# Kernel tuning notes

Measured on AMD Instinct MI355X. Metric: run time of the kernel, lower is better.

The kernel has to match this reference:

```python
import jax, jax.numpy as jnp
import numpy as np

N = 50000       # nodes
E = 800000      # edges (avg degree 16)
D_IN = 96
D_OUT = 96
K = 3           # Chebyshev order
EPS = 1e-5      # BatchNorm eps


def setup_inputs() -> dict:
    key = jax.random.key(0)
    k1, k2, k3 = jax.random.split(key, 3)
    x = jax.random.normal(k1, (N, D_IN), dtype=jnp.float32)
    edge_index = jax.random.randint(k2, (2, E), 0, N)
    # ChebConv weights: one [D_IN, D_OUT] matrix per Chebyshev order + shared bias
    W = jax.random.normal(k3, (K, D_IN, D_OUT), dtype=jnp.float32) * (1.0 / np.sqrt(D_IN))
    bias = jnp.zeros((D_OUT,), dtype=jnp.float32)
    # BatchNorm1d affine params
    gamma = jnp.ones((D_OUT,), dtype=jnp.float32)
    beta = jnp.zeros((D_OUT,), dtype=jnp.float32)
    return {"x": x, "edge_index": edge_index, "W": W, "bias": bias,
            "gamma": gamma, "beta": beta}


def _cheb_edge_norm(edge_index, num_nodes):
    # PyG ChebConv.__norm__ with normalization='sym', lambda_max=2.0:
    # L_hat = 2L/lambda_max - I = -D^{-1/2} A D^{-1/2} (self loops removed, diag 0)
    row, col = edge_index[0], edge_index[1]
    w = jnp.where(row != col, 1.0, 0.0)  # remove self loops (weight 0 == removed)
    deg = jax.ops.segment_sum(w, row, num_segments=num_nodes)
    dis = jnp.where(deg > 0, jax.lax.rsqrt(jnp.maximum(deg, 1e-12)), 0.0)
    return -dis[row] * w * dis[col]  # [E]


def reference(x, edge_index, W, bias, gamma, beta):
    row, col = edge_index[0], edge_index[1]
    norm = _cheb_edge_norm(edge_index, N)

    def prop(h):  # sparse L_hat @ h via gather + scatter-add
        return jax.ops.segment_sum(norm[:, None] * h[row], col, num_segments=N)

    # Chebyshev recursion: T0 = x, T1 = L_hat x, Tk = 2 L_hat T_{k-1} - T_{k-2}
    Tx0 = x
    out = Tx0 @ W[0]
    Tx1 = prop(Tx0)
    out = out + Tx1 @ W[1]
    for k in range(2, K):
        Tx2 = 2.0 * prop(Tx1) - Tx0
        out = out + Tx2 @ W[k]
        Tx0, Tx1 = Tx1, Tx2
    out = out + bias

    # BatchNorm1d (training mode: batch stats over nodes, biased variance)
    mean = out.mean(axis=0)
    var = out.var(axis=0)
    return (out - mean) * jax.lax.rsqrt(var + EPS) * gamma + beta
```

## Files before the change

### kernel.cpp

```cpp
#include <hip/hip_runtime.h>

#define N_NODES 50000
#define N_EDGES 800000
#define D 96
#define DH 48
#define CAP 48
#define HG 64
#define W4 (N_NODES / 4)
#define EPS_BN 1e-5f

typedef short bf16x8 __attribute__((ext_vector_type(8)));
typedef float f32x4  __attribute__((ext_vector_type(4)));
union frag_cvt { uint4 u; bf16x8 f; };

__device__ __forceinline__ unsigned pack_bf16(float a, float b) {
    unsigned ua = __float_as_uint(a), ub = __float_as_uint(b);
    ua = (ua + 0x7fffu + ((ua >> 16) & 1u)) >> 16;
    ub = (ub + 0x7fffu + ((ub >> 16) & 1u)) >> 16;
    return (ua & 0xffffu) | (ub << 16);
}
__device__ __forceinline__ unsigned bf16_hi_bits(float a) {
    unsigned u = __float_as_uint(a);
    return (u + 0x7fffu + ((u >> 16) & 1u)) & 0xffff0000u;
}
__device__ __forceinline__ float bf16_lo(unsigned u) { return __uint_as_float(u << 16); }
__device__ __forceinline__ float bf16_hi(unsigned u) { return __uint_as_float(u & 0xffff0000u); }

#define CB ((N_NODES * DH + 1023) / 1024)
__global__ __launch_bounds__(1024) void prep_hist_kernel(
        const int* __restrict__ ei, unsigned* __restrict__ rowpart,
        unsigned* __restrict__ colpart, const float* __restrict__ x,
        unsigned* __restrict__ xh, const float* __restrict__ W,
        unsigned* __restrict__ wswz) {
    if (blockIdx.x < HG) {
        __shared__ unsigned h[W4];
        const int chunk = N_EDGES / HG;
        const int e0 = blockIdx.x * chunk;
        int rs[13], cs[13];
        int n = 0;
        for (int e = e0 + threadIdx.x; e < e0 + chunk; e += 1024, ++n) {
            rs[n] = ei[e];
            cs[n] = ei[N_EDGES + e];
        }
        for (int w = threadIdx.x; w < W4; w += 1024) h[w] = 0;
        __syncthreads();
        for (int i = 0; i < n; ++i)
            if (rs[i] != cs[i]) atomicAdd(&h[rs[i] >> 2], 1u << ((rs[i] & 3) * 8));
        __syncthreads();
        unsigned* rp = rowpart + (size_t)blockIdx.x * W4;
        for (int w = threadIdx.x; w < W4; w += 1024) rp[w] = h[w];
        __syncthreads();
        for (int w = threadIdx.x; w < W4; w += 1024) h[w] = 0;
        __syncthreads();
        for (int i = 0; i < n; ++i)
            if (rs[i] != cs[i]) atomicAdd(&h[cs[i] >> 2], 1u << ((cs[i] & 3) * 8));
        __syncthreads();
        unsigned* cp = colpart + (size_t)blockIdx.x * W4;
        for (int w = threadIdx.x; w < W4; w += 1024) cp[w] = h[w];
    } else if (blockIdx.x < HG + CB) {
        int t = (blockIdx.x - HG) * 1024 + threadIdx.x;
        if (t >= N_NODES * DH) return;
        float2 v = ((const float2*)x)[t];
        xh[t] = pack_bf16(v.x, v.y);
    } else {
        int t = (blockIdx.x - HG - CB) * 1024 + threadIdx.x;
        if (t >= 3 * 3 * 6 * 64) return;
        int lane = t & 63;
        int rest = t >> 6;
        int tile = rest % 6; rest /= 6;
        int q    = rest % 3;
        int s    = rest / 3;
        int n     = tile * 16 + (lane & 15);
        int kbase = q * 32 + (lane >> 4) * 8;
        uint4 u;
        const float* Wk = W + ((size_t)s * D + kbase) * D + n;
        u.x = pack_bf16(Wk[0 * D], Wk[1 * D]);
        u.y = pack_bf16(Wk[2 * D], Wk[3 * D]);
        u.z = pack_bf16(Wk[4 * D], Wk[5 * D]);
        u.w = pack_bf16(Wk[6 * D], Wk[7 * D]);
        ((uint4*)wswz)[t] = u;
    }
}

__global__ void reduce_kernel(unsigned* __restrict__ colpart,
                              const unsigned* __restrict__ rowpart,
                              int* __restrict__ cnt, float* __restrict__ dis,
                              float* __restrict__ stats) {
    if (blockIdx.x == 0 && threadIdx.x < 2 * D) stats[threadIdx.x] = 0.f;
    int w = blockIdx.x * blockDim.x + threadIdx.x;
    if (w >= W4) return;
    unsigned run = 0;
    for (int b = 0; b < HG; ++b) {
        unsigned v = colpart[(size_t)b * W4 + w];
        colpart[(size_t)b * W4 + w] = run;
        run += v;
    }
    int4 c4;
    c4.x = run & 0xffu; c4.y = (run >> 8) & 0xffu;
    c4.z = (run >> 16) & 0xffu; c4.w = run >> 24;
    ((int4*)cnt)[w] = c4;
    unsigned s0 = 0, s1 = 0, s2 = 0, s3 = 0;
    for (int b = 0; b < HG; ++b) {
        unsigned v = rowpart[(size_t)b * W4 + w];
        s0 += v & 0xffu; s1 += (v >> 8) & 0xffu;
        s2 += (v >> 16) & 0xffu; s3 += v >> 24;
    }
    float4 o;
    o.x = s0 ? rsqrtf((float)s0) : 0.f;
    o.y = s1 ? rsqrtf((float)s1) : 0.f;
    o.z = s2 ? rsqrtf((float)s2) : 0.f;
    o.w = s3 ? rsqrtf((float)s3) : 0.f;
    ((float4*)dis)[w] = o;
}

__global__ __launch_bounds__(1024) void place_kernel(const int* __restrict__ ei,
                                                     const unsigned* __restrict__ colpart,
                                                     const float* __restrict__ dis,
                                                     unsigned* __restrict__ ent) {
    __shared__ unsigned h[W4];
    const unsigned* pref = colpart + (size_t)blockIdx.x * W4;
    for (int w = threadIdx.x; w < W4; w += 1024) h[w] = pref[w];
    __syncthreads();
    const int chunk = N_EDGES / HG;
    const int e0 = blockIdx.x * chunk;
    for (int e = e0 + threadIdx.x; e < e0 + chunk; e += 1024) {
        int r = ei[e];
        int c = ei[N_EDGES + e];
        if (r == c) continue;
        float w = -dis[r] * dis[c];
        int sh = (c & 3) * 8;
        unsigned old = atomicAdd(&h[c >> 2], 1u << sh);
        int pos = (old >> sh) & 0xff;
        if (pos < CAP) ent[c * CAP + pos] = bf16_hi_bits(w) | (unsigned)r;
    }
}

template <int MODE>
__global__ __launch_bounds__(256) void prop_gather_kernel(
        const int* __restrict__ cnt_arr, const unsigned* __restrict__ ent,
        const unsigned* __restrict__ hp, const float* __restrict__ x,
        unsigned* __restrict__ out_h) {
    int node = blockIdx.x * 4 + (threadIdx.x >> 6);
    int lane = threadIdx.x & 63;
    if (node >= N_NODES) return;
    const int cl = (lane < DH) ? lane : (lane - DH);
    int cnt = cnt_arr[node]; if (cnt > CAP) cnt = CAP;
    unsigned el = (lane < cnt) ? ent[node * CAP + lane] : 0u;
    float acc0 = 0.f, acc1 = 0.f;
    for (int j = 0; j < cnt; j += 24) {
        unsigned ee[24];
        #pragma unroll
        for (int i = 0; i < 24; ++i)
            ee[i] = (unsigned)__shfl((int)el, j + i, 64);
        unsigned uu[24];
        #pragma unroll
        for (int i = 0; i < 24; ++i)
            uu[i] = hp[(ee[i] & 0xffffu) * DH + cl];
        #pragma unroll
        for (int i = 0; i < 24; ++i) {
            float w = __uint_as_float(ee[i] & 0xffff0000u);
            acc0 = fmaf(w, bf16_lo(uu[i]), acc0);
            acc1 = fmaf(w, bf16_hi(uu[i]), acc1);
        }
    }
    if (lane < DH) {
        if (MODE == 0) {
            out_h[node * DH + cl] = pack_bf16(acc0, acc1);
        } else {
            float2 xv = ((const float2*)x)[node * DH + cl];
            out_h[node * DH + cl] = pack_bf16(fmaf(2.f, acc0, -xv.x),
                                              fmaf(2.f, acc1, -xv.y));
        }
    }
}

__global__ __launch_bounds__(256) void mfma_gemm_kernel(
        const unsigned* __restrict__ xh, const unsigned* __restrict__ t1h,
        const unsigned* __restrict__ t2h, const unsigned* __restrict__ wswz,
        const float* __restrict__ bias, float* __restrict__ out,
        float* __restrict__ stats) {
    const int wave = threadIdx.x >> 6;
    const int lane = threadIdx.x & 63;
    const int m    = lane & 15;
    const int kg   = lane >> 4;
    const int nb   = blockIdx.x * 128 + wave * 32;
    __shared__ float ssum[4][D], ssq[4][D];

    int arow0 = nb + m;       if (arow0 > N_NODES - 1) arow0 = N_NODES - 1;
    int arow1 = nb + 16 + m;  if (arow1 > N_NODES - 1) arow1 = N_NODES - 1;

    const unsigned* bases[3] = {xh, t1h, t2h};

    f32x4 acc[2][6];
    #pragma unroll
    for (int h = 0; h < 2; ++h)
        #pragma unroll
        for (int t = 0; t < 6; ++t) acc[h][t] = (f32x4){0.f, 0.f, 0.f, 0.f};

    #pragma unroll
    for (int s = 0; s < 3; ++s) {
        const unsigned* A0 = bases[s] + (size_t)arow0 * DH + kg * 4;
        const unsigned* A1 = bases[s] + (size_t)arow1 * DH + kg * 4;
        #pragma unroll
        for (int q = 0; q < 3; ++q) {
            frag_cvt a0, a1;
            a0.u = *(const uint4*)(A0 + q * 16);
            a1.u = *(const uint4*)(A1 + q * 16);
            const uint4* Bp = (const uint4*)wswz + (size_t)((s * 3 + q) * 6) * 64 + lane;
            #pragma unroll
            for (int t = 0; t < 6; ++t) {
                frag_cvt b;
                b.u = Bp[t * 64];
                acc[0][t] = __builtin_amdgcn_mfma_f32_16x16x32_bf16(a0.f, b.f, acc[0][t], 0, 0, 0);
                acc[1][t] = __builtin_amdgcn_mfma_f32_16x16x32_bf16(a1.f, b.f, acc[1][t], 0, 0, 0);
            }
        }
    }

    #pragma unroll
    for (int t = 0; t < 6; ++t) {
        int col = t * 16 + m;
        float bv = bias[col];
        float s1 = 0.f, s2 = 0.f;
        #pragma unroll
        for (int h = 0; h < 2; ++h) {
            #pragma unroll
            for (int r = 0; r < 4; ++r) {
                int g = nb + h * 16 + kg * 4 + r;
                if (g < N_NODES) {
                    float o = acc[h][t][r] + bv;
                    out[(size_t)g * D + col] = o;
                    s1 += o;
                    s2 += o * o;
                }
            }
        }
        s1 += __shfl_xor(s1, 16, 64); s2 += __shfl_xor(s2, 16, 64);
        s1 += __shfl_xor(s1, 32, 64); s2 += __shfl_xor(s2, 32, 64);
        if (lane < 16) { ssum[wave][col] = s1; ssq[wave][col] = s2; }
    }
    __syncthreads();
    if (threadIdx.x < D) {
        int c = threadIdx.x;
        float s1 = ssum[0][c] + ssum[1][c] + ssum[2][c] + ssum[3][c];
        float s2 = ssq [0][c] + ssq [1][c] + ssq [2][c] + ssq [3][c];
        atomicAdd(&stats[c],     s1);
        atomicAdd(&stats[D + c], s2);
    }
}

__global__ void bn_kernel(float* __restrict__ o, const float* __restrict__ stats,
                          const float* __restrict__ gamma, const float* __restrict__ beta) {
    __shared__ __align__(16) float s_sc[D], s_sh[D];
    if (threadIdx.x < D) {
        int c = threadIdx.x;
        const float invN = 1.f / (float)N_NODES;
        float mean = stats[c] * invN;
        float var  = stats[D + c] * invN - mean * mean;
        float inv  = rsqrtf(fmaxf(var, 0.f) + EPS_BN);
        float sc   = gamma[c] * inv;
        s_sc[c] = sc;
        s_sh[c] = beta[c] - mean * sc;
    }
    __syncthreads();
    int t = blockIdx.x * blockDim.x + threadIdx.x;
    if (t >= N_NODES * (D / 4)) return;
    int c4 = t % (D / 4);
    float4 v  = ((float4*)o)[t];
    float4 sc = *(const float4*)(s_sc + c4 * 4);
    float4 sh = *(const float4*)(s_sh + c4 * 4);
    v.x = fmaf(v.x, sc.x, sh.x);
    v.y = fmaf(v.y, sc.y, sh.y);
    v.z = fmaf(v.z, sc.z, sh.z);
    v.w = fmaf(v.w, sc.w, sh.w);
    ((float4*)o)[t] = v;
}

extern "C" void kernel_launch(void* const* d_in, const int* in_sizes, int n_in,
                              void* d_out, int out_size, void* d_ws, size_t ws_size,
                              hipStream_t stream) {
    const float* x     = (const float*)d_in[0];
    const int*   ei    = (const int*)  d_in[1];
    const float* W     = (const float*)d_in[2];
    const float* bias  = (const float*)d_in[3];
    const float* gamma = (const float*)d_in[4];
    const float* beta  = (const float*)d_in[5];
    float* out = (float*)d_out;

    float*    stats   = (float*)d_ws;
    float*    dis     = stats + 2 * D;
    int*      cnt     = (int*)(dis + N_NODES);
    unsigned* ent     = (unsigned*)(cnt + N_NODES);
    unsigned* xh      = ent + (size_t)N_NODES * CAP;
    unsigned* t1h     = xh  + (size_t)N_NODES * DH;
    unsigned* t2h     = t1h + (size_t)N_NODES * DH;
    unsigned* wswz    = t2h + (size_t)N_NODES * DH;
    unsigned* rowpart = t2h;
    unsigned* colpart = t2h + (size_t)HG * W4;

    prep_hist_kernel<<<HG + CB + 4, 1024, 0, stream>>>(ei, rowpart, colpart,
                                                       x, xh, W, wswz);
    reduce_kernel<<<(W4 + 255) / 256, 256, 0, stream>>>(colpart, rowpart, cnt,
                                                        dis, stats);
    place_kernel<<<HG, 1024, 0, stream>>>(ei, colpart, dis, ent);

    const int prop_blocks = (N_NODES + 3) / 4;
    prop_gather_kernel<0><<<prop_blocks, 256, 0, stream>>>(cnt, ent, xh,  nullptr, t1h);
    prop_gather_kernel<1><<<prop_blocks, 256, 0, stream>>>(cnt, ent, t1h, x,       t2h);

    mfma_gemm_kernel<<<(N_NODES + 127) / 128, 256, 0, stream>>>(
        xh, t1h, t2h, wswz, bias, out, stats);

    bn_kernel<<<(N_NODES * (D / 4) + 255) / 256, 256, 0, stream>>>(out, stats, gamma, beta);
}
```

Baseline: 217.6 us.

## Fuse graph-build stages and GEMM+BatchNorm into cooperative kernels with grid sync

Merges the histogram, reduce and place kernels into one cooperative kernel separated by grid-wide syncs. The place stage reuses the edge indices already held in registers instead of reloading them. The GEMM and BatchNorm kernels are also fused: column statistics are gathered, a grid sync follows, and the normalized result is written straight from the accumulators, so the output is no longer stored, reloaded and rewritten. Bias is dropped because BatchNorm mean subtraction cancels it. The trade-off is grid-sync overhead, plus a need for all blocks to be co-resident, which constrains occupancy and grid size.

```diff
diff --git a/kernel.cpp b/kernel.cpp
--- a/kernel.cpp
+++ b/kernel.cpp
@@ -1,4 +1,7 @@
 #include <hip/hip_runtime.h>
+#include <hip/hip_cooperative_groups.h>
+
+namespace cg = cooperative_groups;
 
 #define N_NODES 50000
 #define N_EDGES 800000
@@ -6,6 +9,7 @@
 #define DH 48
 #define CAP 48
 #define HG 64
+#define TB 256
 #define W4 (N_NODES / 4)
 #define EPS_BN 1e-5f
 
@@ -26,19 +30,22 @@
 __device__ __forceinline__ float bf16_lo(unsigned u) { return __uint_as_float(u << 16); }
 __device__ __forceinline__ float bf16_hi(unsigned u) { return __uint_as_float(u & 0xffff0000u); }
 
-#define CB ((N_NODES * DH + 1023) / 1024)
-__global__ __launch_bounds__(1024) void prep_hist_kernel(
+__global__ __launch_bounds__(1024) void build_kernel(
         const int* __restrict__ ei, unsigned* __restrict__ rowpart,
         unsigned* __restrict__ colpart, const float* __restrict__ x,
         unsigned* __restrict__ xh, const float* __restrict__ W,
-        unsigned* __restrict__ wswz) {
+        unsigned* __restrict__ wswz, int* __restrict__ cnt,
+        float* __restrict__ dis, float* __restrict__ stats,
+        unsigned* __restrict__ ent) {
+    cg::grid_group grid = cg::this_grid();
+    __shared__ unsigned h[W4];
+    int rs[13], cs[13];
+    int n = 0;
+
     if (blockIdx.x < HG) {
-        __shared__ unsigned h[W4];
         const int chunk = N_EDGES / HG;
         const int e0 = blockIdx.x * chunk;
-        int rs[13], cs[13];
-        int n = 0;
-        for (int e = e0 + threadIdx.x; e < e0 + chunk; e += 1024, ++n) {
+        for (int e = e0 + (int)threadIdx.x; e < e0 + chunk; e += 1024, ++n) {
             rs[n] = ei[e];
             cs[n] = ei[N_EDGES + e];
         }
@@ -57,81 +64,76 @@
         __syncthreads();
         unsigned* cp = colpart + (size_t)blockIdx.x * W4;
         for (int w = threadIdx.x; w < W4; w += 1024) cp[w] = h[w];
-    } else if (blockIdx.x < HG + CB) {
-        int t = (blockIdx.x - HG) * 1024 + threadIdx.x;
-        if (t >= N_NODES * DH) return;
-        float2 v = ((const float2*)x)[t];
-        xh[t] = pack_bf16(v.x, v.y);
     } else {
-        int t = (blockIdx.x - HG - CB) * 1024 + threadIdx.x;
-        if (t >= 3 * 3 * 6 * 64) return;
-        int lane = t & 63;
-        int rest = t >> 6;
-        int tile = rest % 6; rest /= 6;
-        int q    = rest % 3;
-        int s    = rest / 3;
-        int n     = tile * 16 + (lane & 15);
-        int kbase = q * 32 + (lane >> 4) * 8;
-        uint4 u;
-        const float* Wk = W + ((size_t)s * D + kbase) * D + n;
-        u.x = pack_bf16(Wk[0 * D], Wk[1 * D]);
-        u.y = pack_bf16(Wk[2 * D], Wk[3 * D]);
-        u.z = pack_bf16(Wk[4 * D], Wk[5 * D]);
-        u.w = pack_bf16(Wk[6 * D], Wk[7 * D]);
-        ((uint4*)wswz)[t] = u;
-    }
-}
-
-__global__ void reduce_kernel(unsigned* __restrict__ colpart,
-                              const unsigned* __restrict__ rowpart,
-                              int* __restrict__ cnt, float* __restrict__ dis,
-                              float* __restrict__ stats) {
-    if (blockIdx.x == 0 && threadIdx.x < 2 * D) stats[threadIdx.x] = 0.f;
-    int w = blockIdx.x * blockDim.x + threadIdx.x;
-    if (w >= W4) return;
-    unsigned run = 0;
-    for (int b = 0; b < HG; ++b) {
-        unsigned v = colpart[(size_t)b * W4 + w];
-        colpart[(size_t)b * W4 + w] = run;
-        run += v;
-    }
-    int4 c4;
-    c4.x = run & 0xffu; c4.y = (run >> 8) & 0xffu;
-    c4.z = (run >> 16) & 0xffu; c4.w = run >> 24;
-    ((int4*)cnt)[w] = c4;
-    unsigned s0 = 0, s1 = 0, s2 = 0, s3 = 0;
-    for (int b = 0; b < HG; ++b) {
-        unsigned v = rowpart[(size_t)b * W4 + w];
-        s0 += v & 0xffu; s1 += (v >> 8) & 0xffu;
-        s2 += (v >> 16) & 0xffu; s3 += v >> 24;
-    }
-    float4 o;
-    o.x = s0 ? rsqrtf((float)s0) : 0.f;
-    o.y = s1 ? rsqrtf((float)s1) : 0.f;
-    o.z = s2 ? rsqrtf((float)s2) : 0.f;
-    o.w = s3 ? rsqrtf((float)s3) : 0.f;
-    ((float4*)dis)[w] = o;
-}
-
-__global__ __launch_bounds__(1024) void place_kernel(const int* __restrict__ ei,
-                                                     const unsigned* __restrict__ colpart,
-                                                     const float* __restrict__ dis,
-                                                     unsigned* __restrict__ ent) {
-    __shared__ unsigned h[W4];
-    const unsigned* pref = colpart + (size_t)blockIdx.x * W4;
-    for (int w = threadIdx.x; w < W4; w += 1024) h[w] = pref[w];
-    __syncthreads();
-    const int chunk = N_EDGES / HG;
-    const int e0 = blockIdx.x * chunk;
-    for (int e = e0 + threadIdx.x; e < e0 + chunk; e += 1024) {
-        int r = ei[e];
-        int c = ei[N_EDGES + e];
-        if (r == c) continue;
-        float w = -dis[r] * dis[c];
-        int sh = (c & 3) * 8;
-        unsigned old = atomicAdd(&h[c >> 2], 1u << sh);
-        int pos = (old >> sh) & 0xff;
-        if (pos < CAP) ent[c * CAP + pos] = bf16_hi_bits(w) | (unsigned)r;
+        int T = (blockIdx.x - HG) * 1024 + (int)threadIdx.x;
+        for (int t = T; t < N_NODES * DH; t += (TB - HG) * 1024) {
+            float2 v = ((const float2*)x)[t];
+            xh[t] = pack_bf16(v.x, v.y);
+        }
+        if (T < 3 * 3 * 6 * 64) {
+            int lane = T & 63;
+            int rest = T >> 6;
+            int tile = rest % 6; rest /= 6;
+            int q    = rest % 3;
+            int s    = rest / 3;
+            int nn    = tile * 16 + (lane & 15);
+            int kbase = q * 32 + (lane >> 4) * 8;
+            uint4 u;
+            const float* Wk = W + ((size_t)s * D + kbase) * D + nn;
+            u.x = pack_bf16(Wk[0 * D], Wk[1 * D]);
+            u.y = pack_bf16(Wk[2 * D], Wk[3 * D]);
+            u.z = pack_bf16(Wk[4 * D], Wk[5 * D]);
+            u.w = pack_bf16(Wk[6 * D], Wk[7 * D]);
+            ((uint4*)wswz)[T] = u;
+        }
+        if (T < 2 * D) stats[T] = 0.f;
+    }
+
+    grid.sync();
+
+    if (blockIdx.x >= HG) {
+        int w = (blockIdx.x - HG) * 1024 + (int)threadIdx.x;
+        if (w < W4) {
+            unsigned run = 0;
+            for (int b = 0; b < HG; ++b) {
+                unsigned v = colpart[(size_t)b * W4 + w];
+                colpart[(size_t)b * W4 + w] = run;
+                run += v;
+            }
+            int4 c4;
+            c4.x = run & 0xffu; c4.y = (run >> 8) & 0xffu;
+            c4.z = (run >> 16) & 0xffu; c4.w = run >> 24;
+            ((int4*)cnt)[w] = c4;
+            unsigned s0 = 0, s1 = 0, s2 = 0, s3 = 0;
+            for (int b = 0; b < HG; ++b) {
+                unsigned v = rowpart[(size_t)b * W4 + w];
+                s0 += v & 0xffu; s1 += (v >> 8) & 0xffu;
+                s2 += (v >> 16) & 0xffu; s3 += v >> 24;
+            }
+            float4 o;
+            o.x = s0 ? rsqrtf((float)s0) : 0.f;
+            o.y = s1 ? rsqrtf((float)s1) : 0.f;
+            o.z = s2 ? rsqrtf((float)s2) : 0.f;
+            o.w = s3 ? rsqrtf((float)s3) : 0.f;
+            ((float4*)dis)[w] = o;
+        }
+    }
+
+    grid.sync();
+
+    if (blockIdx.x < HG) {
+        const unsigned* pref = colpart + (size_t)blockIdx.x * W4;
+        for (int w = threadIdx.x; w < W4; w += 1024) h[w] = pref[w];
+        __syncthreads();
+        for (int i = 0; i < n; ++i) {
+            int r = rs[i], c = cs[i];
+            if (r == c) continue;
+            float wgt = -dis[r] * dis[c];
+            int sh = (c & 3) * 8;
+            unsigned old = atomicAdd(&h[c >> 2], 1u << sh);
+            int pos = (old >> sh) & 0xff;
+            if (pos < CAP) ent[c * CAP + pos] = bf16_hi_bits(wgt) | (unsigned)r;
+        }
     }
 }
 
@@ -174,11 +176,12 @@
     }
 }
 
-__global__ __launch_bounds__(256) void mfma_gemm_kernel(
+__global__ __launch_bounds__(256, 2) void gemm_bn_kernel(
         const unsigned* __restrict__ xh, const unsigned* __restrict__ t1h,
         const unsigned* __restrict__ t2h, const unsigned* __restrict__ wswz,
-        const float* __restrict__ bias, float* __restrict__ out,
-        float* __restrict__ stats) {
+        float* __restrict__ out, float* __restrict__ stats,
+        const float* __restrict__ gamma, const float* __restrict__ beta) {
+    cg::grid_group grid = cg::this_grid();
     const int wave = threadIdx.x >> 6;
     const int lane = threadIdx.x & 63;
     const int m    = lane & 15;
@@ -220,7 +223,6 @@
     #pragma unroll
     for (int t = 0; t < 6; ++t) {
         int col = t * 16 + m;
-        float bv = bias[col];
         float s1 = 0.f, s2 = 0.f;
         #pragma unroll
         for (int h = 0; h < 2; ++h) {
@@ -228,8 +230,7 @@
             for (int r = 0; r < 4; ++r) {
                 int g = nb + h * 16 + kg * 4 + r;
                 if (g < N_NODES) {
-                    float o = acc[h][t][r] + bv;
-                    out[(size_t)g * D + col] = o;
+                    float o = acc[h][t][r];
                     s1 += o;
                     s2 += o * o;
                 }
@@ -242,38 +243,32 @@
     __syncthreads();
     if (threadIdx.x < D) {
         int c = threadIdx.x;
-        float s1 = ssum[0][c] + ssum[1][c] + ssum[2][c] + ssum[3][c];
-        float s2 = ssq [0][c] + ssq [1][c] + ssq [2][c] + ssq [3][c];
-        atomicAdd(&stats[c],     s1);
-        atomicAdd(&stats[D + c], s2);
-    }
-}
-
-__global__ void bn_kernel(float* __restrict__ o, const float* __restrict__ stats,
-                          const float* __restrict__ gamma, const float* __restrict__ beta) {
-    __shared__ __align__(16) float s_sc[D], s_sh[D];
-    if (threadIdx.x < D) {
-        int c = threadIdx.x;
-        const float invN = 1.f / (float)N_NODES;
-        float mean = stats[c] * invN;
-        float var  = stats[D + c] * invN - mean * mean;
+        atomicAdd(&stats[c],     ssum[0][c] + ssum[1][c] + ssum[2][c] + ssum[3][c]);
+        atomicAdd(&stats[D + c], ssq [0][c] + ssq [1][c] + ssq [2][c] + ssq [3][c]);
+    }
+    __threadfence();
+
+    grid.sync();
+
+    const float invN = 1.f / (float)N_NODES;
+    #pragma unroll
+    for (int t = 0; t < 6; ++t) {
+        int col = t * 16 + m;
+        float mean = stats[col] * invN;
+        float var  = stats[D + col] * invN - mean * mean;
         float inv  = rsqrtf(fmaxf(var, 0.f) + EPS_BN);
-        float sc   = gamma[c] * inv;
-        s_sc[c] = sc;
-        s_sh[c] = beta[c] - mean * sc;
-    }
-    __syncthreads();
-    int t = blockIdx.x * blockDim.x + threadIdx.x;
-    if (t >= N_NODES * (D / 4)) return;
-    int c4 = t % (D / 4);
-    float4 v  = ((float4*)o)[t];
-    float4 sc = *(const float4*)(s_sc + c4 * 4);
-    float4 sh = *(const float4*)(s_sh + c4 * 4);
-    v.x = fmaf(v.x, sc.x, sh.x);
-    v.y = fmaf(v.y, sc.y, sh.y);
-    v.z = fmaf(v.z, sc.z, sh.z);
-    v.w = fmaf(v.w, sc.w, sh.w);
-    ((float4*)o)[t] = v;
+        float sc   = gamma[col] * inv;
+        float sh   = beta[col] - mean * sc;
+        #pragma unroll
+        for (int h = 0; h < 2; ++h) {
+            #pragma unroll
+            for (int r = 0; r < 4; ++r) {
+                int g = nb + h * 16 + kg * 4 + r;
+                if (g < N_NODES)
+                    out[(size_t)g * D + col] = fmaf(acc[h][t][r], sc, sh);
+            }
+        }
+    }
 }
 
 extern "C" void kernel_launch(void* const* d_in, const int* in_sizes, int n_in,
@@ -286,6 +281,7 @@
     const float* gamma = (const float*)d_in[4];
     const float* beta  = (const float*)d_in[5];
     float* out = (float*)d_out;
+    (void)bias;
 
     float*    stats   = (float*)d_ws;
     float*    dis     = stats + 2 * D;
@@ -298,18 +294,19 @@
     unsigned* rowpart = t2h;
     unsigned* colpart = t2h + (size_t)HG * W4;
 
-    prep_hist_kernel<<<HG + CB + 4, 1024, 0, stream>>>(ei, rowpart, colpart,
-                                                       x, xh, W, wswz);
-    reduce_kernel<<<(W4 + 255) / 256, 256, 0, stream>>>(colpart, rowpart, cnt,
-                                                        dis, stats);
-    place_kernel<<<HG, 1024, 0, stream>>>(ei, colpart, dis, ent);
+    void* bargs[] = {(void*)&ei, (void*)&rowpart, (void*)&colpart, (void*)&x,
+                     (void*)&xh, (void*)&W, (void*)&wswz, (void*)&cnt,
+                     (void*)&dis, (void*)&stats, (void*)&ent};
+    hipLaunchCooperativeKernel((const void*)build_kernel, dim3(TB), dim3(1024),
+                               bargs, 0, stream);
 
     const int prop_blocks = (N_NODES + 3) / 4;
     prop_gather_kernel<0><<<prop_blocks, 256, 0, stream>>>(cnt, ent, xh,  nullptr, t1h);
     prop_gather_kernel<1><<<prop_blocks, 256, 0, stream>>>(cnt, ent, t1h, x,       t2h);
 
-    mfma_gemm_kernel<<<(N_NODES + 127) / 128, 256, 0, stream>>>(
-        xh, t1h, t2h, wswz, bias, out, stats);
-
-    bn_kernel<<<(N_NODES * (D / 4) + 255) / 256, 256, 0, stream>>>(out, stats, gamma, beta);
-}
+    void* gargs[] = {(void*)&xh, (void*)&t1h, (void*)&t2h, (void*)&wswz,
+                     (void*)&out, (void*)&stats, (void*)&gamma, (void*)&beta};
+    hipLaunchCooperativeKernel((const void*)gemm_bn_kernel,
+                               dim3((N_NODES + 127) / 128), dim3(256),
+                               gargs, 0, stream);
+}
```

After: 329.2 us. +51.3%, slower.

## Fuse GEMM and BatchNorm via cooperative grid sync, drop bias add

Applied to the files above, without the earlier changes.

Merges the MFMA GEMM and the BatchNorm pass into one cooperative kernel. Accumulators stay in registers across a grid-wide sync, so the un-normalized output is never written and re-read. The bias add is dropped because training-mode BatchNorm subtracts the batch mean, which cancels any per-column constant. The risk is that the 391-block grid must be co-resident for the cooperative launch (hence launch_bounds 256,2), and the grid sync adds latency.

```diff
diff --git a/kernel.cpp b/kernel.cpp
--- a/kernel.cpp
+++ b/kernel.cpp
@@ -1,4 +1,7 @@
 #include <hip/hip_runtime.h>
+#include <hip/hip_cooperative_groups.h>
+
+namespace cg = cooperative_groups;
 
 #define N_NODES 50000
 #define N_EDGES 800000
@@ -174,11 +177,12 @@
     }
 }
 
-__global__ __launch_bounds__(256) void mfma_gemm_kernel(
+__global__ __launch_bounds__(256, 2) void gemm_bn_kernel(
         const unsigned* __restrict__ xh, const unsigned* __restrict__ t1h,
         const unsigned* __restrict__ t2h, const unsigned* __restrict__ wswz,
-        const float* __restrict__ bias, float* __restrict__ out,
-        float* __restrict__ stats) {
+        float* __restrict__ out, float* __restrict__ stats,
+        const float* __restrict__ gamma, const float* __restrict__ beta) {
+    cg::grid_group grid = cg::this_grid();
     const int wave = threadIdx.x >> 6;
     const int lane = threadIdx.x & 63;
     const int m    = lane & 15;
@@ -220,7 +224,6 @@
     #pragma unroll
     for (int t = 0; t < 6; ++t) {
         int col = t * 16 + m;
-        float bv = bias[col];
         float s1 = 0.f, s2 = 0.f;
         #pragma unroll
         for (int h = 0; h < 2; ++h) {
@@ -228,8 +231,7 @@
             for (int r = 0; r < 4; ++r) {
                 int g = nb + h * 16 + kg * 4 + r;
                 if (g < N_NODES) {
-                    float o = acc[h][t][r] + bv;
-                    out[(size_t)g * D + col] = o;
+                    float o = acc[h][t][r];
                     s1 += o;
                     s2 += o * o;
                 }
@@ -242,38 +244,32 @@
     __syncthreads();
     if (threadIdx.x < D) {
         int c = threadIdx.x;
-        float s1 = ssum[0][c] + ssum[1][c] + ssum[2][c] + ssum[3][c];
-        float s2 = ssq [0][c] + ssq [1][c] + ssq [2][c] + ssq [3][c];
-        atomicAdd(&stats[c],     s1);
-        atomicAdd(&stats[D + c], s2);
-    }
-}
-
-__global__ void bn_kernel(float* __restrict__ o, const float* __restrict__ stats,
-                          const float* __restrict__ gamma, const float* __restrict__ beta) {
-    __shared__ __align__(16) float s_sc[D], s_sh[D];
-    if (threadIdx.x < D) {
-        int c = threadIdx.x;
-        const float invN = 1.f / (float)N_NODES;
-        float mean = stats[c] * invN;
-        float var  = stats[D + c] * invN - mean * mean;
+        atomicAdd(&stats[c],     ssum[0][c] + ssum[1][c] + ssum[2][c] + ssum[3][c]);
+        atomicAdd(&stats[D + c], ssq [0][c] + ssq [1][c] + ssq [2][c] + ssq [3][c]);
+    }
+    __threadfence();
+
+    grid.sync();
+
+    const float invN = 1.f / (float)N_NODES;
+    #pragma unroll
+    for (int t = 0; t < 6; ++t) {
+        int col = t * 16 + m;
+        float mean = stats[col] * invN;
+        float var  = stats[D + col] * invN - mean * mean;
         float inv  = rsqrtf(fmaxf(var, 0.f) + EPS_BN);
-        float sc   = gamma[c] * inv;
-        s_sc[c] = sc;
-        s_sh[c] = beta[c] - mean * sc;
-    }
-    __syncthreads();
-    int t = blockIdx.x * blockDim.x + threadIdx.x;
-    if (t >= N_NODES * (D / 4)) return;
-    int c4 = t % (D / 4);
-    float4 v  = ((float4*)o)[t];
-    float4 sc = *(const float4*)(s_sc + c4 * 4);
-    float4 sh = *(const float4*)(s_sh + c4 * 4);
-    v.x = fmaf(v.x, sc.x, sh.x);
-    v.y = fmaf(v.y, sc.y, sh.y);
-    v.z = fmaf(v.z, sc.z, sh.z);
-    v.w = fmaf(v.w, sc.w, sh.w);
-    ((float4*)o)[t] = v;
+        float sc   = gamma[col] * inv;
+        float sh   = beta[col] - mean * sc;
+        #pragma unroll
+        for (int h = 0; h < 2; ++h) {
+            #pragma unroll
+            for (int r = 0; r < 4; ++r) {
+                int g = nb + h * 16 + kg * 4 + r;
+                if (g < N_NODES)
+                    out[(size_t)g * D + col] = fmaf(acc[h][t][r], sc, sh);
+            }
+        }
+    }
 }
 
 extern "C" void kernel_launch(void* const* d_in, const int* in_sizes, int n_in,
@@ -286,6 +282,7 @@
     const float* gamma = (const float*)d_in[4];
     const float* beta  = (const float*)d_in[5];
     float* out = (float*)d_out;
+    (void)bias;
 
     float*    stats   = (float*)d_ws;
     float*    dis     = stats + 2 * D;
@@ -308,8 +305,9 @@
     prop_gather_kernel<0><<<prop_blocks, 256, 0, stream>>>(cnt, ent, xh,  nullptr, t1h);
     prop_gather_kernel<1><<<prop_blocks, 256, 0, stream>>>(cnt, ent, t1h, x,       t2h);
 
-    mfma_gemm_kernel<<<(N_NODES + 127) / 128, 256, 0, stream>>>(
-        xh, t1h, t2h, wswz, bias, out, stats);
-
-    bn_kernel<<<(N_NODES * (D / 4) + 255) / 256, 256, 0, stream>>>(out, stats, gamma, beta);
-}
+    void* gargs[] = {(void*)&xh, (void*)&t1h, (void*)&t2h, (void*)&wswz,
+                     (void*)&out, (void*)&stats, (void*)&gamma, (void*)&beta};
+    hipLaunchCooperativeKernel((const void*)gemm_bn_kernel,
+                               dim3((N_NODES + 127) / 128), dim3(256),
+                               gargs, 0, stream);
+}
```

Measured after the change: 270.8 us. +24.5%, slower.
